# Kernel optimization log

Measured on AMD Instinct MI355X. Metric: run time of the kernel, lower is better.

Reference implementation:

```python
import jax, jax.numpy as jnp
import numpy as np

B, T, C = 2, 2048, 2048
H, KV, D = 16, 4, 128
G = H // KV  # kv groups
THETA = 10000.0


def setup_inputs() -> dict:
    key = jax.random.key(0)
    ks = jax.random.split(key, 5)
    x = jax.random.normal(ks[0], (B, T, C), dtype=jnp.float32)
    wq = jax.random.normal(ks[1], (H * D, C), dtype=jnp.float32) * 0.02
    wk = jax.random.normal(ks[2], (KV * D, C), dtype=jnp.float32) * 0.02
    wv = jax.random.normal(ks[3], (KV * D, C), dtype=jnp.float32) * 0.02
    wo = jax.random.normal(ks[4], (H * D, C), dtype=jnp.float32).T * 0.02  # [C, H*D] stored as [out,in]
    wo = jnp.asarray(wo)
    # rotary frequencies: freqs_cis = exp(i * t * theta^{-2j/D}) for j in [0, D/2)
    inv_freq = 1.0 / (THETA ** (jnp.arange(0, D, 2, dtype=jnp.float32) / D))  # [D/2]
    angles = jnp.arange(T, dtype=jnp.float32)[:, None] * inv_freq[None, :]    # [T, D/2]
    freqs_cos = jnp.cos(angles)
    freqs_sin = jnp.sin(angles)
    # additive causal mask [1,1,T,T]
    mask = jnp.where(jnp.tril(jnp.ones((T, T), dtype=bool)), 0.0, -1e9).astype(jnp.float32)[None, None]
    return {"x": x, "wq": wq, "wk": wk, "wv": wv, "wo": wo,
            "freqs_cos": freqs_cos, "freqs_sin": freqs_sin, "mask": mask}


def _apply_rope(t, cos, sin):
    # t: [B, T, nH, D]; cos/sin: [T, D/2]
    th = t.reshape(*t.shape[:-1], D // 2, 2)
    t0, t1 = th[..., 0], th[..., 1]
    c = cos[None, :, None, :]
    s = sin[None, :, None, :]
    o0 = t0 * c - t1 * s
    o1 = t0 * s + t1 * c
    return jnp.stack([o0, o1], axis=-1).reshape(t.shape)


def reference(x, wq, wk, wv, wo, freqs_cos, freqs_sin, mask):
    Bx, Tx, Cx = x.shape
    xq = (x @ wq.T).reshape(Bx, Tx, H, D)
    xk = (x @ wk.T).reshape(Bx, Tx, KV, D)
    xv = (x @ wv.T).reshape(Bx, Tx, KV, D)
    xq = _apply_rope(xq, freqs_cos, freqs_sin)
    xk = _apply_rope(xk, freqs_cos, freqs_sin)
    # GQA: repeat_interleave KV heads to match query heads
    xk = jnp.repeat(xk, G, axis=2)  # [B, T, H, D]
    xv = jnp.repeat(xv, G, axis=2)
    # [B, H, T, D]
    xq = xq.transpose(0, 2, 1, 3)
    xk = xk.transpose(0, 2, 1, 3)
    xv = xv.transpose(0, 2, 1, 3)
    scores = jnp.einsum('bhqd,bhkd->bhqk', xq, xk) / jnp.sqrt(jnp.float32(D))
    scores = scores + mask
    probs = jax.nn.softmax(scores.astype(jnp.float32), axis=-1).astype(xq.dtype)
    out = jnp.einsum('bhqk,bhkd->bhqd', probs, xv)
    out = out.transpose(0, 2, 1, 3).reshape(Bx, Tx, H * D)
    return out @ wo.T
```

## Files before the change

kernel.cpp:

```cpp
#include <hip/hip_runtime.h>
#include <hip/hip_bf16.h>

typedef __bf16 bf16_t;
typedef __bf16 bf16x8 __attribute__((ext_vector_type(8)));
typedef __bf16 bf16x4 __attribute__((ext_vector_type(4)));
typedef float f32x4 __attribute__((ext_vector_type(4)));
typedef float f32x16 __attribute__((ext_vector_type(16)));

#define SCALE_Q2 0.12752518895325724f

__device__ __forceinline__ void gload_lds16(const void* g, void* l) {
  __builtin_amdgcn_global_load_lds(
      (const __attribute__((address_space(1))) void*)g,
      (__attribute__((address_space(3))) void*)l, 16, 0, 0);
}

__global__ __launch_bounds__(256) void cvt_all(
    const float* __restrict__ x, const float* __restrict__ wq,
    const float* __restrict__ wk, const float* __restrict__ wv,
    const float* __restrict__ wo, bf16_t* __restrict__ xb,
    bf16_t* __restrict__ wqkv, bf16_t* __restrict__ wo_b) {
  int i = blockIdx.x * 256 + threadIdx.x;
  const int stride = gridDim.x * 256;
  for (; i < 4718592; i += stride) {
    const int e = i * 4;
    const float* src;
    bf16_t* dst;
    if (e < 8388608) {
      src = x + e;              dst = xb + e;
    } else if (e < 12582912) {
      src = wq + (e - 8388608); dst = wqkv + (e - 8388608);
    } else if (e < 13631488) {
      src = wk + (e - 12582912); dst = wqkv + (e - 8388608);
    } else if (e < 14680064) {
      src = wv + (e - 13631488); dst = wqkv + (e - 8388608);
    } else {
      src = wo + (e - 14680064); dst = wo_b + (e - 14680064);
    }
    f32x4 v = *reinterpret_cast<const f32x4*>(src);
    bf16x4 r;
    r[0] = (bf16_t)v[0]; r[1] = (bf16_t)v[1];
    r[2] = (bf16_t)v[2]; r[3] = (bf16_t)v[3];
    *reinterpret_cast<bf16x4*>(dst) = r;
  }
}

template <typename OutT>
__global__ __launch_bounds__(256) void gemm_bt(
    const bf16_t* __restrict__ A, const bf16_t* __restrict__ W,
    OutT* __restrict__ C, int M, int N, int K) {
  __shared__ bf16_t As[128 * 32];
  __shared__ bf16_t Ws[128 * 32];
  const int tid = threadIdx.x;
  const int lane = tid & 63;
  const int wid = tid >> 6;
  const int wr = wid >> 1, wc = wid & 1;
  const int l15 = lane & 15, lg = lane >> 4;
  const int r0 = blockIdx.y * 128;
  const int c0 = blockIdx.x * 128;

  f32x4 acc[4][4];
#pragma unroll
  for (int mi = 0; mi < 4; ++mi)
#pragma unroll
    for (int ni = 0; ni < 4; ++ni)
#pragma unroll
      for (int j = 0; j < 4; ++j) acc[mi][ni][j] = 0.f;

  for (int k0 = 0; k0 < K; k0 += 32) {
#pragma unroll
    for (int s = 0; s < 2; ++s) {
      const int chunk = wid * 2 + s;
      const int eoff = (chunk * 64 + lane) * 8;
      const int r = eoff >> 5, c = eoff & 31;
      gload_lds16(A + (size_t)(r0 + r) * K + k0 + c, (char*)As + chunk * 1024);
      gload_lds16(W + (size_t)(c0 + r) * K + k0 + c, (char*)Ws + chunk * 1024);
    }
    __syncthreads();
    bf16x8 af[4], wf[4];
#pragma unroll
    for (int mi = 0; mi < 4; ++mi)
      af[mi] = *reinterpret_cast<const bf16x8*>(
          &As[(wr * 64 + mi * 16 + l15) * 32 + lg * 8]);
#pragma unroll
    for (int ni = 0; ni < 4; ++ni)
      wf[ni] = *reinterpret_cast<const bf16x8*>(
          &Ws[(wc * 64 + ni * 16 + l15) * 32 + lg * 8]);
#pragma unroll
    for (int mi = 0; mi < 4; ++mi)
#pragma unroll
      for (int ni = 0; ni < 4; ++ni)
        acc[mi][ni] = __builtin_amdgcn_mfma_f32_16x16x32_bf16(
            af[mi], wf[ni], acc[mi][ni], 0, 0, 0);
    __syncthreads();
  }

#pragma unroll
  for (int mi = 0; mi < 4; ++mi)
#pragma unroll
    for (int ni = 0; ni < 4; ++ni)
#pragma unroll
      for (int j = 0; j < 4; ++j) {
        const int row = r0 + wr * 64 + mi * 16 + lg * 4 + j;
        const int col = c0 + wc * 64 + ni * 16 + l15;
        const float v = acc[mi][ni][j];
        if constexpr (__is_same(OutT, float))
          C[(size_t)row * N + col] = v;
        else
          C[(size_t)row * N + col] = (bf16_t)v;
      }
}

__global__ __launch_bounds__(256) void rope_layout(
    const bf16_t* __restrict__ qkv, const float* __restrict__ fc,
    const float* __restrict__ fs, bf16_t* __restrict__ Qr,
    bf16_t* __restrict__ Kr) {
  const int n = blockIdx.x;
  const int b = n >> 11, t = n & 2047;
  const int tid = threadIdx.x;
  const bf16_t* row = qkv + (size_t)n * 3072;

#pragma unroll
  for (int i = 0; i < 4; ++i) {
    const int p = i * 256 + tid;
    const int h = p >> 6, j = p & 63;
    const float t0 = (float)row[h * 128 + 2 * j];
    const float t1 = (float)row[h * 128 + 2 * j + 1];
    const float c = fc[t * 64 + j], s = fs[t * 64 + j];
    const size_t dst = ((size_t)(b * 16 + h) * 2048 + t) * 128 + 2 * j;
    Qr[dst] = (bf16_t)((t0 * c - t1 * s) * SCALE_Q2);
    Qr[dst + 1] = (bf16_t)((t0 * s + t1 * c) * SCALE_Q2);
  }
  {
    const int kvh = tid >> 6, j = tid & 63;
    const float t0 = (float)row[2048 + kvh * 128 + 2 * j];
    const float t1 = (float)row[2048 + kvh * 128 + 2 * j + 1];
    const float c = fc[t * 64 + j], s = fs[t * 64 + j];
    const size_t dst = ((size_t)(b * 4 + kvh) * 2048 + t) * 128 + 2 * j;
    Kr[dst] = (bf16_t)(t0 * c - t1 * s);
    Kr[dst + 1] = (bf16_t)(t0 * s + t1 * c);
  }
}

__global__ __launch_bounds__(256) void v_trans(
    const bf16_t* __restrict__ qkv, bf16_t* __restrict__ Vt) {
  __shared__ bf16_t L[64][68];
  const int bid = blockIdx.x;
  const int tt = bid & 31;
  const int dt2 = (bid >> 5) & 1;
  const int bk = bid >> 6;
  const int b = bk >> 2, kvh = bk & 3;
  const int t0 = tt * 64, d0 = dt2 * 64;
  const int r = threadIdx.x >> 4;
  const int c4 = (threadIdx.x & 15) * 4;

#pragma unroll
  for (int it = 0; it < 4; ++it) {
    const int tl = r + it * 16;
    const int tp = (tl & ~15) |
                   ((tl & 3) | ((tl & 4) << 1) | ((tl & 8) >> 1));
    const bf16_t* src = qkv + (size_t)(b * 2048 + t0 + tl) * 3072 + 2560 +
                        kvh * 128 + d0 + c4;
    *reinterpret_cast<bf16x4*>(&L[tp][c4]) =
        *reinterpret_cast<const bf16x4*>(src);
  }
  __syncthreads();
#pragma unroll
  for (int it = 0; it < 4; ++it) {
    const int dr = r + it * 16;
    bf16x4 v;
#pragma unroll
    for (int j = 0; j < 4; ++j) v[j] = L[c4 + j][dr];
    *reinterpret_cast<bf16x4*>(Vt + ((size_t)bk * 128 + d0 + dr) * 2048 +
                               t0 + c4) = v;
  }
}

#define VLOAD(buf, kf, kc)                                               \
  {                                                                      \
    _Pragma("unroll") for (int dtile_ = 0; dtile_ < 4; ++dtile_)         \
        buf[dtile_] = *reinterpret_cast<const bf16x8*>(                  \
            Vbase + (size_t)(dtile_ * 32 + l31) * 2048 + k0 + (kf) * 32 +\
            (kc) * 16 + hi * 8);                                         \
  }

__global__ __launch_bounds__(256, 2) void attn_fwd(
    const bf16_t* __restrict__ Qr, const bf16_t* __restrict__ Kr,
    const bf16_t* __restrict__ Vt, bf16_t* __restrict__ Oout) {
  __shared__ __align__(16) bf16_t Klds[2][128 * 128];
  const int tid = threadIdx.x;
  const int lane = tid & 63, w = tid >> 6;
  const int l31 = lane & 31, hi = lane >> 5;
  const int sidx = blockIdx.x >> 5;
  const int hb = blockIdx.x & 31;
  const int h = hb & 15, b = hb >> 4;
  const int kvh = h >> 2;
  const int st = (sidx < 8) ? (15 - sidx) : (sidx - 8);

  const bf16_t* Kbase = Kr + ((size_t)(b * 4 + kvh) * 2048) * 128;
  const bf16_t* Vbase = Vt + ((size_t)(b * 4 + kvh) * 128) * 2048;

  const int qbw = st * 128 + w * 32;
  const bf16_t* Qbase = Qr + ((size_t)(b * 16 + h) * 2048 + qbw + l31) * 128;

  auto STAGE = [&](bf16_t* dst, int kt) {
    const int k0s = kt * 128;
#pragma unroll
    for (int i = 0; i < 8; ++i) {
      const int c = i * 256 + tid;
      const int row = c >> 4;
      const int col = c & 15;
      const int scol = col ^ (row & 15);
      gload_lds16(Kbase + (size_t)(k0s + row) * 128 + scol * 8, dst + c * 8);
    }
  };

  STAGE(&Klds[0][0], 0);

  bf16x8 qf[8];
#pragma unroll
  for (int dt = 0; dt < 8; ++dt)
    qf[dt] = *reinterpret_cast<const bf16x8*>(Qbase + dt * 16 + hi * 8);

  f32x16 o[4];
#pragma unroll
  for (int d = 0; d < 4; ++d)
#pragma unroll
    for (int r = 0; r < 16; ++r) o[d][r] = 0.f;
  float lsum = 0.f;

  const int nt = st + 1;
  int cur = 0;
  for (int kt = 0; kt < nt; ++kt) {
    const int k0 = kt * 128;
    const bool last = (kt == nt - 1);
    const int kfmax = last ? w : 3;

    bf16x8 vaA[4], vaB[4];
    VLOAD(vaA, 0, 0);
    VLOAD(vaB, 0, 1);

    __syncthreads();
    if (kt + 1 < nt) STAGE(&Klds[cur ^ 1][0], kt + 1);

    const char* KB = (const char*)&Klds[cur][0];

#pragma unroll
    for (int kp = 0; kp < 2; ++kp) {
      f32x16 sA, sB;
      __builtin_amdgcn_s_setprio(1);
      if (2 * kp <= kfmax) {
#pragma unroll
        for (int r = 0; r < 16; ++r) sA[r] = 0.f;
#pragma unroll
        for (int dt = 0; dt < 8; ++dt) {
          const int boff = ((2 * kp) * 32 + l31) * 256 +
                           ((dt * 32 + hi * 16) ^ ((l31 & 15) << 4));
          bf16x8 ka = *reinterpret_cast<const bf16x8*>(KB + boff);
          sA = __builtin_amdgcn_mfma_f32_32x32x16_bf16(ka, qf[dt], sA, 0, 0, 0);
        }
      }
      if (2 * kp + 1 <= kfmax) {
#pragma unroll
        for (int r = 0; r < 16; ++r) sB[r] = 0.f;
#pragma unroll
        for (int dt = 0; dt < 8; ++dt) {
          const int boff = ((2 * kp + 1) * 32 + l31) * 256 +
                           ((dt * 32 + hi * 16) ^ ((l31 & 15) << 4));
          bf16x8 ka = *reinterpret_cast<const bf16x8*>(KB + boff);
          sB = __builtin_amdgcn_mfma_f32_32x32x16_bf16(ka, qf[dt], sB, 0, 0, 0);
        }
      }
      __builtin_amdgcn_s_setprio(0);

#pragma unroll
      for (int ki = 0; ki < 2; ++ki) {
        const int kf = 2 * kp + ki;
        if (kf <= kfmax) {
          const bool diag = last && (kf == w);
          float p[16];
#pragma unroll
          for (int r = 0; r < 16; ++r) {
            float e = exp2f(ki ? sB[r] : sA[r]);
            if (diag) {
              const int crow = (r & 3) + 8 * (r >> 2) + 4 * hi;
              if (crow > l31) e = 0.f;
            }
            p[r] = e;
          }
          const float t0 = (p[0] + p[1]) + (p[2] + p[3]);
          const float t1 = (p[4] + p[5]) + (p[6] + p[7]);
          const float t2 = (p[8] + p[9]) + (p[10] + p[11]);
          const float t3 = (p[12] + p[13]) + (p[14] + p[15]);
          lsum += (t0 + t1) + (t2 + t3);

          {
            unsigned int u0, u1, u2, u3;
            asm("v_cvt_pk_bf16_f32 %0, %1, %2" : "=v"(u0)
                : "v"(p[0]), "v"(p[1]));
            asm("v_cvt_pk_bf16_f32 %0, %1, %2" : "=v"(u1)
                : "v"(p[2]), "v"(p[3]));
            asm("v_cvt_pk_bf16_f32 %0, %1, %2" : "=v"(u2)
                : "v"(p[4]), "v"(p[5]));
            asm("v_cvt_pk_bf16_f32 %0, %1, %2" : "=v"(u3)
                : "v"(p[6]), "v"(p[7]));
            union { unsigned int u[4]; bf16x8 v; } pb;
            pb.u[0] = u0; pb.u[1] = u1; pb.u[2] = u2; pb.u[3] = u3;
            __builtin_amdgcn_s_setprio(1);
#pragma unroll
            for (int dtile = 0; dtile < 4; ++dtile)
              o[dtile] = __builtin_amdgcn_mfma_f32_32x32x16_bf16(
                  vaA[dtile], pb.v, o[dtile], 0, 0, 0);
            __builtin_amdgcn_s_setprio(0);
          }
          if (kf < kfmax) VLOAD(vaA, kf + 1, 0);

          {
            unsigned int u0, u1, u2, u3;
            asm("v_cvt_pk_bf16_f32 %0, %1, %2" : "=v"(u0)
                : "v"(p[8]), "v"(p[9]));
            asm("v_cvt_pk_bf16_f32 %0, %1, %2" : "=v"(u1)
                : "v"(p[10]), "v"(p[11]));
            asm("v_cvt_pk_bf16_f32 %0, %1, %2" : "=v"(u2)
                : "v"(p[12]), "v"(p[13]));
            asm("v_cvt_pk_bf16_f32 %0, %1, %2" : "=v"(u3)
                : "v"(p[14]), "v"(p[15]));
            union { unsigned int u[4]; bf16x8 v; } pb;
            pb.u[0] = u0; pb.u[1] = u1; pb.u[2] = u2; pb.u[3] = u3;
            __builtin_amdgcn_s_setprio(1);
#pragma unroll
            for (int dtile = 0; dtile < 4; ++dtile)
              o[dtile] = __builtin_amdgcn_mfma_f32_32x32x16_bf16(
                  vaB[dtile], pb.v, o[dtile], 0, 0, 0);
            __builtin_amdgcn_s_setprio(0);
          }
          if (kf < kfmax) VLOAD(vaB, kf + 1, 1);
        }
      }
    }
    cur ^= 1;
  }

  const float ltot = lsum + __shfl_xor(lsum, 32);
  const float inv = 1.f / ltot;
  bf16_t* Obase = Oout + ((size_t)b * 2048 + qbw + l31) * 2048 + h * 128;
#pragma unroll
  for (int dtile = 0; dtile < 4; ++dtile)
#pragma unroll
    for (int g = 0; g < 4; ++g) {
      bf16x4 stv;
#pragma unroll
      for (int j = 0; j < 4; ++j)
        stv[j] = (bf16_t)(o[dtile][g * 4 + j] * inv);
      *reinterpret_cast<bf16x4*>(Obase + dtile * 32 + 8 * g + 4 * hi) = stv;
    }
}

extern "C" void kernel_launch(void* const* d_in, const int* in_sizes, int n_in,
                              void* d_out, int out_size, void* d_ws,
                              size_t ws_size, hipStream_t stream) {
  const float* x  = (const float*)d_in[0];
  const float* wq = (const float*)d_in[1];
  const float* wk = (const float*)d_in[2];
  const float* wv = (const float*)d_in[3];
  const float* wo = (const float*)d_in[4];
  const float* fc = (const float*)d_in[5];
  const float* fs = (const float*)d_in[6];
  float* out = (float*)d_out;

  char* ws = (char*)d_ws;
  bf16_t* xb      = (bf16_t*)(ws + 0);
  bf16_t* wqkv    = (bf16_t*)(ws + 16777216);
  bf16_t* wo_b    = (bf16_t*)(ws + 29360128);
  bf16_t* qkv     = (bf16_t*)(ws + 37748736);
  bf16_t* Qr      = (bf16_t*)(ws + 62914560);
  bf16_t* Kr      = (bf16_t*)(ws + 79691776);
  bf16_t* Vt      = (bf16_t*)(ws + 83886080);
  bf16_t* attn_o  = xb;

  const int M = 4096;

  cvt_all<<<2048, 256, 0, stream>>>(x, wq, wk, wv, wo, xb, wqkv, wo_b);

  gemm_bt<bf16_t><<<dim3(3072 / 128, M / 128), 256, 0, stream>>>(
      xb, wqkv, qkv, M, 3072, 2048);

  rope_layout<<<4096, 256, 0, stream>>>(qkv, fc, fs, Qr, Kr);
  v_trans<<<512, 256, 0, stream>>>(qkv, Vt);

  attn_fwd<<<512, 256, 0, stream>>>(Qr, Kr, Vt, attn_o);

  gemm_bt<float><<<dim3(2048 / 128, M / 128), 256, 0, stream>>>(
      attn_o, wo_b, out, M, 2048, 2048);
}
```

Before: 240.2 us.

## Double GEMM K-tile to 64 with XOR-swizzled LDS, reorder attention staging

The projection GEMM now loads 64-wide K tiles per barrier pair instead of 32. It stores them in LDS with an XOR swizzle on 16-byte chunks to avoid bank conflicts on the fragment reads, which halves the number of syncs per K. In the attention kernel, the barrier and next-tile K staging are moved ahead of the V register loads so the async copy issues earlier. This doubles GEMM LDS use, which may reduce occupancy.

```diff
diff --git a/kernel.cpp b/kernel.cpp
--- a/kernel.cpp
+++ b/kernel.cpp
@@ -49,8 +49,8 @@
 __global__ __launch_bounds__(256) void gemm_bt(
     const bf16_t* __restrict__ A, const bf16_t* __restrict__ W,
     OutT* __restrict__ C, int M, int N, int K) {
-  __shared__ bf16_t As[128 * 32];
-  __shared__ bf16_t Ws[128 * 32];
+  __shared__ __align__(16) bf16_t As[128 * 64];
+  __shared__ __align__(16) bf16_t Ws[128 * 64];
   const int tid = threadIdx.x;
   const int lane = tid & 63;
   const int wid = tid >> 6;
@@ -67,31 +67,40 @@
 #pragma unroll
       for (int j = 0; j < 4; ++j) acc[mi][ni][j] = 0.f;
 
-  for (int k0 = 0; k0 < K; k0 += 32) {
-#pragma unroll
-    for (int s = 0; s < 2; ++s) {
-      const int chunk = wid * 2 + s;
-      const int eoff = (chunk * 64 + lane) * 8;
-      const int r = eoff >> 5, c = eoff & 31;
-      gload_lds16(A + (size_t)(r0 + r) * K + k0 + c, (char*)As + chunk * 1024);
-      gload_lds16(W + (size_t)(c0 + r) * K + k0 + c, (char*)Ws + chunk * 1024);
+  for (int k0 = 0; k0 < K; k0 += 64) {
+#pragma unroll
+    for (int s = 0; s < 4; ++s) {
+      const int c = s * 256 + tid;
+      const int row = c >> 3;
+      const int scol = (c & 7) ^ (row & 7);
+      gload_lds16(A + (size_t)(r0 + row) * K + k0 + scol * 8,
+                  (char*)As + c * 16);
+      gload_lds16(W + (size_t)(c0 + row) * K + k0 + scol * 8,
+                  (char*)Ws + c * 16);
     }
     __syncthreads();
-    bf16x8 af[4], wf[4];
-#pragma unroll
-    for (int mi = 0; mi < 4; ++mi)
-      af[mi] = *reinterpret_cast<const bf16x8*>(
-          &As[(wr * 64 + mi * 16 + l15) * 32 + lg * 8]);
-#pragma unroll
-    for (int ni = 0; ni < 4; ++ni)
-      wf[ni] = *reinterpret_cast<const bf16x8*>(
-          &Ws[(wc * 64 + ni * 16 + l15) * 32 + lg * 8]);
-#pragma unroll
-    for (int mi = 0; mi < 4; ++mi)
-#pragma unroll
-      for (int ni = 0; ni < 4; ++ni)
-        acc[mi][ni] = __builtin_amdgcn_mfma_f32_16x16x32_bf16(
-            af[mi], wf[ni], acc[mi][ni], 0, 0, 0);
+#pragma unroll
+    for (int kk = 0; kk < 2; ++kk) {
+      bf16x8 af[4], wf[4];
+#pragma unroll
+      for (int mi = 0; mi < 4; ++mi) {
+        const int r = wr * 64 + mi * 16 + l15;
+        af[mi] = *reinterpret_cast<const bf16x8*>(
+            (char*)As + r * 128 + ((kk * 64 + lg * 16) ^ ((r & 7) << 4)));
+      }
+#pragma unroll
+      for (int ni = 0; ni < 4; ++ni) {
+        const int r = wc * 64 + ni * 16 + l15;
+        wf[ni] = *reinterpret_cast<const bf16x8*>(
+            (char*)Ws + r * 128 + ((kk * 64 + lg * 16) ^ ((r & 7) << 4)));
+      }
+#pragma unroll
+      for (int mi = 0; mi < 4; ++mi)
+#pragma unroll
+        for (int ni = 0; ni < 4; ++ni)
+          acc[mi][ni] = __builtin_amdgcn_mfma_f32_16x16x32_bf16(
+              af[mi], wf[ni], acc[mi][ni], 0, 0, 0);
+    }
     __syncthreads();
   }
 
@@ -236,14 +245,14 @@
     const bool last = (kt == nt - 1);
     const int kfmax = last ? w : 3;
 
+    __syncthreads();
+    if (kt + 1 < nt) STAGE(&Klds[cur ^ 1][0], kt + 1);
+
+    const char* KB = (const char*)&Klds[cur][0];
+
     bf16x8 vaA[4], vaB[4];
     VLOAD(vaA, 0, 0);
     VLOAD(vaB, 0, 1);
-
-    __syncthreads();
-    if (kt + 1 < nt) STAGE(&Klds[cur ^ 1][0], kt + 1);
-
-    const char* KB = (const char*)&Klds[cur][0];
 
 #pragma unroll
     for (int kp = 0; kp < 2; ++kp) {
```

Measured after the change: 213.1 us. 1.13x faster.
